# Kernel optimization log

Measured on AMD Instinct MI355X. Metric: run time of the kernel, lower is better.

The kernel has to match this reference:

```python
import jax, jax.numpy as jnp
import numpy as np

B, N, C, H = 2, 512, 64, 8

def setup_inputs() -> dict:
    key = jax.random.key(0)
    k1, k2, k3, k4, k5 = jax.random.split(key, 5)
    query = jax.random.normal(k1, (B, N, N, C), dtype=jnp.float32)
    key_t = jax.random.normal(k2, (B, N, N, C), dtype=jnp.float32)
    roi_mask = jax.random.uniform(k3, (B, N, N), dtype=jnp.float32)
    W = jax.random.normal(k4, (H, 2 * C), dtype=jnp.float32) * (1.0 / np.sqrt(2 * C))
    b = jax.random.normal(k5, (H,), dtype=jnp.float32) * 0.01
    return {"query": query, "key": key_t, "roi_mask": roi_mask, "W": W, "b": b}

def reference(query, key, roi_mask, W, b):
    # ft = cat(query, key) along feature dim -> [B, N, N, 2C]
    # small GEMM: scores [B, N, N, H]; split the matmul to avoid materializing concat
    Wq, Wk = W[:, :C], W[:, C:]  # [H, C] each
    attn = jnp.einsum('bmnc,hc->bmnh', query, Wq) \
         + jnp.einsum('bmnc,hc->bmnh', key, Wk) + b
    attn = jnp.exp(attn) * roi_mask[:, :, :, None]
    attn_sum = attn.sum(axis=2)  # [B, N, H]
    return attn / attn_sum[:, :, None, :]
```

## Files before the change

kernel.cpp:

```cpp
#include <hip/hip_runtime.h>
#include <math.h>

constexpr int BDIM = 512;
constexpr int NDIM = 512;
constexpr int CDIM = 64;
constexpr int HDIM = 8;
constexpr int NWAVE = BDIM / 64;

__global__ __launch_bounds__(BDIM, 8)
void mha_kernel(const float* __restrict__ q,
                const float* __restrict__ kk,
                const float* __restrict__ mask,
                const float* __restrict__ W,
                const float* __restrict__ bias,
                float* __restrict__ out)
{
    __shared__ float red[NWAVE * HDIM];
    __shared__ float rsum_lds[HDIM];

    const int bm = blockIdx.x;
    const int t  = threadIdx.x;
    const int n  = t;

    const float* qrow = q  + (size_t)bm * NDIM * CDIM;
    const float* krow = kk + (size_t)bm * NDIM * CDIM;

    float acc[HDIM];
#pragma unroll
    for (int h = 0; h < HDIM; ++h) acc[h] = 0.0f;

    {
        const float4* qp = (const float4*)(qrow + (size_t)n * CDIM);
        float x[CDIM];
#pragma unroll
        for (int j = 0; j < 16; ++j) {
            float4 v = qp[j];
            x[4 * j + 0] = v.x; x[4 * j + 1] = v.y;
            x[4 * j + 2] = v.z; x[4 * j + 3] = v.w;
        }
#pragma unroll
        for (int h = 0; h < HDIM; ++h) {
            const float* wq = W + h * 2 * CDIM;
            float a = acc[h];
#pragma unroll
            for (int c = 0; c < CDIM; ++c)
                a = fmaf(x[c], wq[c], a);
            acc[h] = a;
        }
    }

    {
        const float4* kp = (const float4*)(krow + (size_t)n * CDIM);
        float x[CDIM];
#pragma unroll
        for (int j = 0; j < 16; ++j) {
            float4 v = kp[j];
            x[4 * j + 0] = v.x; x[4 * j + 1] = v.y;
            x[4 * j + 2] = v.z; x[4 * j + 3] = v.w;
        }
#pragma unroll
        for (int h = 0; h < HDIM; ++h) {
            const float* wk = W + h * 2 * CDIM + CDIM;
            float a = acc[h];
#pragma unroll
            for (int c = 0; c < CDIM; ++c)
                a = fmaf(x[c], wk[c], a);
            acc[h] = a;
        }
    }

    const float mval = mask[bm * NDIM + n];
    float val[HDIM];
    float psum[HDIM];
#pragma unroll
    for (int h = 0; h < HDIM; ++h) {
        float v = __expf(acc[h] + bias[h]) * mval;
        val[h]  = v;
        psum[h] = v;
    }

#pragma unroll
    for (int h = 0; h < HDIM; ++h) {
        float s = psum[h];
#pragma unroll
        for (int off = 32; off >= 1; off >>= 1)
            s += __shfl_xor(s, off, 64);
        psum[h] = s;
    }
    const int lane = t & 63;
    const int wid  = t >> 6;
    if (lane == 0) {
#pragma unroll
        for (int h = 0; h < HDIM; ++h) red[wid * HDIM + h] = psum[h];
    }
    __syncthreads();
    if (t < HDIM) {
        float s = 0.0f;
#pragma unroll
        for (int w = 0; w < NWAVE; ++w) s += red[w * HDIM + t];
        rsum_lds[t] = 1.0f / s;
    }
    __syncthreads();

    float rs[HDIM];
#pragma unroll
    for (int h = 0; h < HDIM; ++h) rs[h] = rsum_lds[h];

    float* orow = out + (size_t)bm * NDIM * HDIM;
    float4 lo = make_float4(val[0] * rs[0], val[1] * rs[1],
                            val[2] * rs[2], val[3] * rs[3]);
    float4 hi = make_float4(val[4] * rs[4], val[5] * rs[5],
                            val[6] * rs[6], val[7] * rs[7]);
    float4* op = (float4*)(orow + (size_t)n * HDIM);
    op[0] = lo;
    op[1] = hi;
}

extern "C" void kernel_launch(void* const* d_in, const int* in_sizes, int n_in,
                              void* d_out, int out_size, void* d_ws, size_t ws_size,
                              hipStream_t stream) {
    const float* q    = (const float*)d_in[0];
    const float* k    = (const float*)d_in[1];
    const float* mask = (const float*)d_in[2];
    const float* W    = (const float*)d_in[3];
    const float* b    = (const float*)d_in[4];
    float* out = (float*)d_out;

    hipLaunchKernelGGL(mha_kernel, dim3(2 * NDIM), dim3(BDIM), 0, stream,
                       q, k, mask, W, b, out);
}
```

Baseline: 293.6 us.

## Remap threads to (row-group, head, chunk) lanes with per-head dot products

Replaces the one-thread-per-row mapping, where each thread held 64-element q/k rows and computed all 8 heads, with a layout where 4 lanes split the channel dimension of one head for a row and each thread walks 32 consecutive rows. Weights stay in registers, partial dot products are combined with two lane shuffles, and the softmax denominator is reduced per head through a small LDS array. The aim is to cut register pressure from the large per-thread arrays and to make each wave's loads contiguous 64B segments. In exchange, each q/k element is loaded redundantly by 8 head lanes (relying on cache broadcast), and output stores become scalar strided writes from only a quarter of the threads. Launch bounds are lowered from 8 to 4 blocks.

```diff
diff --git a/kernel.cpp b/kernel.cpp
--- a/kernel.cpp
+++ b/kernel.cpp
@@ -6,8 +6,9 @@
 constexpr int CDIM = 64;
 constexpr int HDIM = 8;
 constexpr int NWAVE = BDIM / 64;
+constexpr int RPT   = 32;
 
-__global__ __launch_bounds__(BDIM, 8)
+__global__ __launch_bounds__(BDIM, 4)
 void mha_kernel(const float* __restrict__ q,
                 const float* __restrict__ kk,
                 const float* __restrict__ mask,
@@ -16,104 +17,80 @@
                 float* __restrict__ out)
 {
     __shared__ float red[NWAVE * HDIM];
-    __shared__ float rsum_lds[HDIM];
 
-    const int bm = blockIdx.x;
-    const int t  = threadIdx.x;
-    const int n  = t;
+    const int bm     = blockIdx.x;
+    const int t      = threadIdx.x;
+    const int chunk  = t & 3;
+    const int head   = (t >> 2) & 7;
+    const int rowgrp = t >> 5;
+    const int row0   = rowgrp << 5;
 
-    const float* qrow = q  + (size_t)bm * NDIM * CDIM;
-    const float* krow = kk + (size_t)bm * NDIM * CDIM;
+    float4 wq4[4], wk4[4];
+#pragma unroll
+    for (int j = 0; j < 4; ++j) {
+        wq4[j] = *(const float4*)(W + head * 2 * CDIM + j * 16 + chunk * 4);
+        wk4[j] = *(const float4*)(W + head * 2 * CDIM + CDIM + j * 16 + chunk * 4);
+    }
+    const float bh = bias[head];
 
-    float acc[HDIM];
+    const float* qb = q    + (size_t)bm * NDIM * CDIM;
+    const float* kb = kk   + (size_t)bm * NDIM * CDIM;
+    const float* mb = mask + (size_t)bm * NDIM;
+
+    float vals[RPT];
+    float psum = 0.0f;
+
 #pragma unroll
-    for (int h = 0; h < HDIM; ++h) acc[h] = 0.0f;
+    for (int k = 0; k < RPT; ++k) {
+        const int row = row0 + k;
+        const float4* qp = (const float4*)(qb + (size_t)row * CDIM);
+        const float4* kp = (const float4*)(kb + (size_t)row * CDIM);
 
-    {
-        const float4* qp = (const float4*)(qrow + (size_t)n * CDIM);
-        float x[CDIM];
+        float s = 0.0f;
 #pragma unroll
-        for (int j = 0; j < 16; ++j) {
-            float4 v = qp[j];
-            x[4 * j + 0] = v.x; x[4 * j + 1] = v.y;
-            x[4 * j + 2] = v.z; x[4 * j + 3] = v.w;
+        for (int j = 0; j < 4; ++j) {
+            float4 xq = qp[j * 4 + chunk];
+            s = fmaf(xq.x, wq4[j].x, s);
+            s = fmaf(xq.y, wq4[j].y, s);
+            s = fmaf(xq.z, wq4[j].z, s);
+            s = fmaf(xq.w, wq4[j].w, s);
         }
 #pragma unroll
-        for (int h = 0; h < HDIM; ++h) {
-            const float* wq = W + h * 2 * CDIM;
-            float a = acc[h];
-#pragma unroll
-            for (int c = 0; c < CDIM; ++c)
-                a = fmaf(x[c], wq[c], a);
-            acc[h] = a;
+        for (int j = 0; j < 4; ++j) {
+            float4 xk = kp[j * 4 + chunk];
+            s = fmaf(xk.x, wk4[j].x, s);
+            s = fmaf(xk.y, wk4[j].y, s);
+            s = fmaf(xk.z, wk4[j].z, s);
+            s = fmaf(xk.w, wk4[j].w, s);
         }
+        s += __shfl_xor(s, 1, 64);
+        s += __shfl_xor(s, 2, 64);
+
+        const float v = __expf(s + bh) * mb[row];
+        vals[k] = v;
+        psum += v;
     }
 
-    {
-        const float4* kp = (const float4*)(krow + (size_t)n * CDIM);
-        float x[CDIM];
-#pragma unroll
-        for (int j = 0; j < 16; ++j) {
-            float4 v = kp[j];
-            x[4 * j + 0] = v.x; x[4 * j + 1] = v.y;
-            x[4 * j + 2] = v.z; x[4 * j + 3] = v.w;
-        }
-#pragma unroll
-        for (int h = 0; h < HDIM; ++h) {
-            const float* wk = W + h * 2 * CDIM + CDIM;
-            float a = acc[h];
-#pragma unroll
-            for (int c = 0; c < CDIM; ++c)
-                a = fmaf(x[c], wk[c], a);
-            acc[h] = a;
-        }
-    }
+    float tot = psum * 4.0f;
+    tot += __shfl_xor(tot, 32, 64);
 
-    const float mval = mask[bm * NDIM + n];
-    float val[HDIM];
-    float psum[HDIM];
-#pragma unroll
-    for (int h = 0; h < HDIM; ++h) {
-        float v = __expf(acc[h] + bias[h]) * mval;
-        val[h]  = v;
-        psum[h] = v;
-    }
-
-#pragma unroll
-    for (int h = 0; h < HDIM; ++h) {
-        float s = psum[h];
-#pragma unroll
-        for (int off = 32; off >= 1; off >>= 1)
-            s += __shfl_xor(s, off, 64);
-        psum[h] = s;
-    }
     const int lane = t & 63;
     const int wid  = t >> 6;
-    if (lane == 0) {
-#pragma unroll
-        for (int h = 0; h < HDIM; ++h) red[wid * HDIM + h] = psum[h];
-    }
-    __syncthreads();
-    if (t < HDIM) {
-        float s = 0.0f;
-#pragma unroll
-        for (int w = 0; w < NWAVE; ++w) s += red[w * HDIM + t];
-        rsum_lds[t] = 1.0f / s;
-    }
+    if (lane < 32 && (lane & 3) == 0)
+        red[wid * HDIM + (lane >> 2)] = tot;
     __syncthreads();
 
-    float rs[HDIM];
+    float total = 0.0f;
 #pragma unroll
-    for (int h = 0; h < HDIM; ++h) rs[h] = rsum_lds[h];
+    for (int w2 = 0; w2 < NWAVE; ++w2) total += red[w2 * HDIM + head];
+    const float rinv = 4.0f / total;
 
-    float* orow = out + (size_t)bm * NDIM * HDIM;
-    float4 lo = make_float4(val[0] * rs[0], val[1] * rs[1],
-                            val[2] * rs[2], val[3] * rs[3]);
-    float4 hi = make_float4(val[4] * rs[4], val[5] * rs[5],
-                            val[6] * rs[6], val[7] * rs[7]);
-    float4* op = (float4*)(orow + (size_t)n * HDIM);
-    op[0] = lo;
-    op[1] = hi;
+    float* ob = out + (size_t)bm * NDIM * HDIM;
+    if (chunk == 0) {
+#pragma unroll
+        for (int k = 0; k < RPT; ++k)
+            ob[(size_t)(row0 + k) * HDIM + head] = vals[k] * rinv;
+    }
 }
 
 extern "C" void kernel_launch(void* const* d_in, const int* in_sizes, int n_in,
```

Result: slower. 445.5 us (+51.8%).

## Stage q/k rows through swizzled LDS tiles for coalesced global loads

Applied to the files above, without the earlier changes.

Each wave now loads 64-float slices of 64 rows cooperatively, with groups of four lanes covering one row's 16-column chunk, so the global reads are coalesced. The data is written to a per-wave LDS tile with an XOR swizzle to avoid bank conflicts, and each lane then reads back its own row. This replaces the old pattern of one thread streaming one 256-byte row, and it also lowers register pressure by not holding 64 floats per thread. It adds LDS traffic and changes launch bounds from 8 to 6. No barrier is needed because the tile is private to each wave.

```diff
diff --git a/kernel.cpp b/kernel.cpp
--- a/kernel.cpp
+++ b/kernel.cpp
@@ -7,7 +7,7 @@
 constexpr int HDIM = 8;
 constexpr int NWAVE = BDIM / 64;
 
-__global__ __launch_bounds__(BDIM, 8)
+__global__ __launch_bounds__(BDIM, 6)
 void mha_kernel(const float* __restrict__ q,
                 const float* __restrict__ kk,
                 const float* __restrict__ mask,
@@ -15,61 +15,68 @@
                 const float* __restrict__ bias,
                 float* __restrict__ out)
 {
+    __shared__ float4 tile[NWAVE][64][4];
     __shared__ float red[NWAVE * HDIM];
     __shared__ float rsum_lds[HDIM];
 
-    const int bm = blockIdx.x;
-    const int t  = threadIdx.x;
-    const int n  = t;
+    const int bm   = blockIdx.x;
+    const int t    = threadIdx.x;
+    const int lane = t & 63;
+    const int wid  = t >> 6;
 
-    const float* qrow = q  + (size_t)bm * NDIM * CDIM;
-    const float* krow = kk + (size_t)bm * NDIM * CDIM;
+    const float* qb = q  + (size_t)bm * NDIM * CDIM;
+    const float* kb = kk + (size_t)bm * NDIM * CDIM;
+
+    const int srow = lane >> 2;
+    const int sj   = lane & 3;
 
     float acc[HDIM];
 #pragma unroll
     for (int h = 0; h < HDIM; ++h) acc[h] = 0.0f;
 
-    {
-        const float4* qp = (const float4*)(qrow + (size_t)n * CDIM);
-        float x[CDIM];
+    const int rsw = (lane >> 1) & 3;
+
 #pragma unroll
-        for (int j = 0; j < 16; ++j) {
-            float4 v = qp[j];
-            x[4 * j + 0] = v.x; x[4 * j + 1] = v.y;
-            x[4 * j + 2] = v.z; x[4 * j + 3] = v.w;
+    for (int p = 0; p < 8; ++p) {
+        const float* src = (p < 4) ? qb : kb;
+        const int slice  = p & 3;
+        const float* srcw = src + (size_t)(wid * 64) * CDIM + slice * 16 + sj * 4;
+        float4 g0 = *(const float4*)(srcw + (size_t)(srow +  0) * CDIM);
+        float4 g1 = *(const float4*)(srcw + (size_t)(srow + 16) * CDIM);
+        float4 g2 = *(const float4*)(srcw + (size_t)(srow + 32) * CDIM);
+        float4 g3 = *(const float4*)(srcw + (size_t)(srow + 48) * CDIM);
+        {
+            const int r0 = srow,      c0 = sj ^ ((r0 >> 1) & 3);
+            const int r1 = srow + 16, c1 = sj ^ ((r1 >> 1) & 3);
+            const int r2 = srow + 32, c2 = sj ^ ((r2 >> 1) & 3);
+            const int r3 = srow + 48, c3 = sj ^ ((r3 >> 1) & 3);
+            tile[wid][r0][c0] = g0;
+            tile[wid][r1][c1] = g1;
+            tile[wid][r2][c2] = g2;
+            tile[wid][r3][c3] = g3;
         }
+        float4 x0 = tile[wid][lane][0 ^ rsw];
+        float4 x1 = tile[wid][lane][1 ^ rsw];
+        float4 x2 = tile[wid][lane][2 ^ rsw];
+        float4 x3 = tile[wid][lane][3 ^ rsw];
+        const float* wbase = W + (p >= 4 ? CDIM : 0) + slice * 16;
 #pragma unroll
         for (int h = 0; h < HDIM; ++h) {
-            const float* wq = W + h * 2 * CDIM;
+            const float* wh = wbase + h * 2 * CDIM;
             float a = acc[h];
-#pragma unroll
-            for (int c = 0; c < CDIM; ++c)
-                a = fmaf(x[c], wq[c], a);
+            a = fmaf(x0.x, wh[0],  a); a = fmaf(x0.y, wh[1],  a);
+            a = fmaf(x0.z, wh[2],  a); a = fmaf(x0.w, wh[3],  a);
+            a = fmaf(x1.x, wh[4],  a); a = fmaf(x1.y, wh[5],  a);
+            a = fmaf(x1.z, wh[6],  a); a = fmaf(x1.w, wh[7],  a);
+            a = fmaf(x2.x, wh[8],  a); a = fmaf(x2.y, wh[9],  a);
+            a = fmaf(x2.z, wh[10], a); a = fmaf(x2.w, wh[11], a);
+            a = fmaf(x3.x, wh[12], a); a = fmaf(x3.y, wh[13], a);
+            a = fmaf(x3.z, wh[14], a); a = fmaf(x3.w, wh[15], a);
             acc[h] = a;
         }
     }
 
-    {
-        const float4* kp = (const float4*)(krow + (size_t)n * CDIM);
-        float x[CDIM];
-#pragma unroll
-        for (int j = 0; j < 16; ++j) {
-            float4 v = kp[j];
-            x[4 * j + 0] = v.x; x[4 * j + 1] = v.y;
-            x[4 * j + 2] = v.z; x[4 * j + 3] = v.w;
-        }
-#pragma unroll
-        for (int h = 0; h < HDIM; ++h) {
-            const float* wk = W + h * 2 * CDIM + CDIM;
-            float a = acc[h];
-#pragma unroll
-            for (int c = 0; c < CDIM; ++c)
-                a = fmaf(x[c], wk[c], a);
-            acc[h] = a;
-        }
-    }
-
-    const float mval = mask[bm * NDIM + n];
+    const float mval = mask[bm * NDIM + t];
     float val[HDIM];
     float psum[HDIM];
 #pragma unroll
@@ -87,8 +94,6 @@
             s += __shfl_xor(s, off, 64);
         psum[h] = s;
     }
-    const int lane = t & 63;
-    const int wid  = t >> 6;
     if (lane == 0) {
 #pragma unroll
         for (int h = 0; h < HDIM; ++h) red[wid * HDIM + h] = psum[h];
@@ -111,7 +116,7 @@
                             val[2] * rs[2], val[3] * rs[3]);
     float4 hi = make_float4(val[4] * rs[4], val[5] * rs[5],
                             val[6] * rs[6], val[7] * rs[7]);
-    float4* op = (float4*)(orow + (size_t)n * HDIM);
+    float4* op = (float4*)(orow + (size_t)t * HDIM);
     op[0] = lo;
     op[1] = hi;
 }
```

Measured after the change: 292.7 us. About the same (-0.3%).
